# Kernel optimization log

Measured on AMD Instinct MI355X. Metric: run time of the kernel, lower is better.

The kernel has to match this reference:

```python
import jax, jax.numpy as jnp
import numpy as np


def setup_inputs() -> dict:
    key = jax.random.key(0)
    ks = jax.random.split(key, 6)
    B, N, D_in, D, Dg, H = 32, 256, 512, 256, 256, 512
    s = lambda f_in: 1.0 / np.sqrt(f_in)
    return {
        "xi": jax.random.normal(ks[0], (B, N, D_in), dtype=jnp.float32),
        "W_img": jax.random.normal(ks[1], (D_in, D), dtype=jnp.float32) * s(D_in),
        "b_img": jnp.zeros((D,), jnp.float32),
        "W_gnn_self": jax.random.normal(ks[2], (D, Dg), dtype=jnp.float32) * s(D),
        "W_gnn_nbr": jax.random.normal(ks[3], (D, Dg), dtype=jnp.float32) * s(D),
        "b_gnn": jnp.zeros((Dg,), jnp.float32),
        "W1": jax.random.normal(ks[4], (N * Dg, H), dtype=jnp.float32) * s(N * Dg),
        "b1": jnp.zeros((H,), jnp.float32),
        "W2": jax.random.normal(ks[5], (H, 1), dtype=jnp.float32) * s(H),
        "b2": jnp.zeros((1,), jnp.float32),
        "k": 10,
    }


def _knn_edges(xie, k):
    # xie: [B, N, D]. Per-image squared euclidean cdist + top-k (exclude self).
    B, N, _ = xie.shape
    x2 = jnp.sum(xie * xie, axis=-1)  # [B, N]
    d2 = x2[:, :, None] + x2[:, None, :] - 2.0 * jnp.einsum("bnd,bmd->bnm", xie, xie)
    big = jnp.asarray(1e30, d2.dtype)
    d2 = d2 + big * jnp.eye(N, dtype=d2.dtype)  # exclude self
    _, nbr = jax.lax.top_k(-d2, k)  # [B, N, k] neighbor (source) indices
    tgt = jnp.broadcast_to(jnp.arange(N)[None, :, None], (B, N, k))
    return nbr, tgt


def reference(xi, W_img, b_img, W_gnn_self, W_gnn_nbr, b_gnn, W1, b1, W2, b2, k):
    B, N, _ = xi.shape
    # image encoder -> per-node embeddings [B, N, D]
    xie = xi @ W_img + b_img
    # KNN graph build per image, then shift indices into one batched graph
    nbr, tgt = _knn_edges(xie, k)
    shift = (jnp.arange(B) * N)[:, None, None]
    src = (nbr + shift).reshape(-1)  # [B*N*k]
    dst = (tgt + shift).reshape(-1)  # [B*N*k]
    # batched graph conv: mean neighbor aggregation + self transform
    x_flat = xie.reshape(B * N, -1)
    agg = jax.ops.segment_sum(x_flat[src], dst, num_segments=B * N) / k
    gep = jax.nn.relu(x_flat @ W_gnn_self + agg @ W_gnn_nbr + b_gnn)
    gep = gep.reshape(B, N, -1)  # split_batch_graph
    # estimation MLP on flattened graph embedding
    h = jax.nn.relu(gep.reshape(B, -1) @ W1 + b1)
    out = h @ W2 + b2  # [B, 1]
    return xie, gep, out
```

## Files before the change

kernel.cpp:

```cpp
#include <hip/hip_runtime.h>

#define BB 32
#define NN 256
#define DIN 512
#define DD 256
#define HH 512
#define MM 8192
#define KSTR 16

typedef __attribute__((ext_vector_type(8))) __bf16 bf16x8;
typedef __attribute__((ext_vector_type(4))) float f32x4;
typedef unsigned short ushort_t;

__device__ __forceinline__ unsigned short f2bf(float x) {
  unsigned u = __float_as_uint(x);
  u += 0x7FFFu + ((u >> 16) & 1u);
  return (unsigned short)(u >> 16);
}

__global__ __launch_bounds__(512) void k_enc(const float* __restrict__ A,
                                             const float* __restrict__ W,
                                             const float* __restrict__ bias,
                                             float* __restrict__ C,
                                             ushort_t* __restrict__ A_bf) {
  __shared__ float Asm[32][520];
  const int tid = threadIdx.x;
  const int mb0 = blockIdx.x * 32;
  const int cg = tid & 31;
  const int mh = (tid >> 5) & 7;
  const int team = tid >> 8;
#pragma unroll
  for (int i = 0; i < 8; ++i) {
    int idx = tid + i * 512;
    int m = idx >> 7;
    int kq = idx & 127;
    float4 v = *reinterpret_cast<const float4*>(&A[(size_t)(mb0 + m) * DIN + kq * 4]);
    *reinterpret_cast<float4*>(&Asm[m][kq * 4]) = v;
  }
  __syncthreads();
  float4 acc[4][2] = {};
  const int kt0 = team * 256;
  const float* wp = &W[(size_t)kt0 * DD + cg * 8];
  float4 wA[4][2], wB[4][2];
#pragma unroll
  for (int j = 0; j < 4; ++j) {
    wA[j][0] = *reinterpret_cast<const float4*>(&wp[(size_t)j * DD]);
    wA[j][1] = *reinterpret_cast<const float4*>(&wp[(size_t)j * DD + 4]);
  }
  for (int it = 0; it < 64; ++it) {
    if (it < 63) {
#pragma unroll
      for (int j = 0; j < 4; ++j) {
        wB[j][0] = *reinterpret_cast<const float4*>(&wp[(size_t)((it + 1) * 4 + j) * DD]);
        wB[j][1] = *reinterpret_cast<const float4*>(&wp[(size_t)((it + 1) * 4 + j) * DD + 4]);
      }
    }
    const int kk = kt0 + it * 4;
#pragma unroll
    for (int r = 0; r < 4; ++r) {
      float4 a = *reinterpret_cast<const float4*>(&Asm[mh * 4 + r][kk]);
#pragma unroll
      for (int h = 0; h < 2; ++h) {
        acc[r][h].x += a.x * wA[0][h].x; acc[r][h].y += a.x * wA[0][h].y;
        acc[r][h].z += a.x * wA[0][h].z; acc[r][h].w += a.x * wA[0][h].w;
        acc[r][h].x += a.y * wA[1][h].x; acc[r][h].y += a.y * wA[1][h].y;
        acc[r][h].z += a.y * wA[1][h].z; acc[r][h].w += a.y * wA[1][h].w;
        acc[r][h].x += a.z * wA[2][h].x; acc[r][h].y += a.z * wA[2][h].y;
        acc[r][h].z += a.z * wA[2][h].z; acc[r][h].w += a.z * wA[2][h].w;
        acc[r][h].x += a.w * wA[3][h].x; acc[r][h].y += a.w * wA[3][h].y;
        acc[r][h].z += a.w * wA[3][h].z; acc[r][h].w += a.w * wA[3][h].w;
      }
    }
#pragma unroll
    for (int j = 0; j < 4; ++j) {
      wA[j][0] = wB[j][0]; wA[j][1] = wB[j][1];
    }
  }
  __syncthreads();
  float* red = &Asm[0][0];
  if (team == 1) {
#pragma unroll
    for (int r = 0; r < 4; ++r) {
      *reinterpret_cast<float4*>(&red[(mh * 4 + r) * 256 + cg * 8]) = acc[r][0];
      *reinterpret_cast<float4*>(&red[(mh * 4 + r) * 256 + cg * 8 + 4]) = acc[r][1];
    }
  }
  __syncthreads();
  if (team == 0) {
    float4 bv0 = *reinterpret_cast<const float4*>(&bias[cg * 8]);
    float4 bv1 = *reinterpret_cast<const float4*>(&bias[cg * 8 + 4]);
#pragma unroll
    for (int r = 0; r < 4; ++r) {
      const int row = mb0 + mh * 4 + r;
      float4 o0 = *reinterpret_cast<float4*>(&red[(mh * 4 + r) * 256 + cg * 8]);
      float4 o1 = *reinterpret_cast<float4*>(&red[(mh * 4 + r) * 256 + cg * 8 + 4]);
      float4 s0, s1;
      s0.x = acc[r][0].x + o0.x + bv0.x; s0.y = acc[r][0].y + o0.y + bv0.y;
      s0.z = acc[r][0].z + o0.z + bv0.z; s0.w = acc[r][0].w + o0.w + bv0.w;
      s1.x = acc[r][1].x + o1.x + bv1.x; s1.y = acc[r][1].y + o1.y + bv1.y;
      s1.z = acc[r][1].z + o1.z + bv1.z; s1.w = acc[r][1].w + o1.w + bv1.w;
      *reinterpret_cast<float4*>(&C[(size_t)row * DD + cg * 8]) = s0;
      *reinterpret_cast<float4*>(&C[(size_t)row * DD + cg * 8 + 4]) = s1;
      ushort4 ob0, ob1;
      ob0.x = f2bf(s0.x); ob0.y = f2bf(s0.y); ob0.z = f2bf(s0.z); ob0.w = f2bf(s0.w);
      ob1.x = f2bf(s1.x); ob1.y = f2bf(s1.y); ob1.z = f2bf(s1.z); ob1.w = f2bf(s1.w);
      *reinterpret_cast<ushort4*>(&A_bf[(size_t)row * 512 + cg * 8]) = ob0;
      *reinterpret_cast<ushort4*>(&A_bf[(size_t)row * 512 + cg * 8 + 4]) = ob1;
    }
  }
}

__global__ __launch_bounds__(256) void k_norm(const float* __restrict__ X,
                                              float* __restrict__ x2) {
  const int tid = threadIdx.x;
  const int row = blockIdx.x * 4 + (tid >> 6);
  const int lane = tid & 63;
  float4 v = *reinterpret_cast<const float4*>(&X[(size_t)row * DD + lane * 4]);
  float s = v.x * v.x + v.y * v.y + v.z * v.z + v.w * v.w;
#pragma unroll
  for (int off = 1; off < 64; off <<= 1) s += __shfl_xor(s, off);
  if (lane == 0) x2[row] = s;
}

__global__ __launch_bounds__(256) void k_dist(const float* __restrict__ X,
                                              const float* __restrict__ x2,
                                              float* __restrict__ d2) {
  __shared__ float As[16][68];
  __shared__ float Bs[16][68];
  const int tid = threadIdx.x;
  const int b = blockIdx.z;
  const int m0 = blockIdx.x * 64, n0 = blockIdx.y * 64;
  const float* Xb = X + b * NN * DD;
  const int tx = tid & 15, ty = tid >> 4;
  const int lrow = tid >> 2, lfc = (tid & 3) * 4;
  float acc[4][4] = {};
  for (int k0 = 0; k0 < DD; k0 += 16) {
    float4 va = *reinterpret_cast<const float4*>(&Xb[(n0 + lrow) * DD + k0 + lfc]);
    As[lfc + 0][lrow] = va.x; As[lfc + 1][lrow] = va.y;
    As[lfc + 2][lrow] = va.z; As[lfc + 3][lrow] = va.w;
    float4 vb = *reinterpret_cast<const float4*>(&Xb[(m0 + lrow) * DD + k0 + lfc]);
    Bs[lfc + 0][lrow] = vb.x; Bs[lfc + 1][lrow] = vb.y;
    Bs[lfc + 2][lrow] = vb.z; Bs[lfc + 3][lrow] = vb.w;
    __syncthreads();
#pragma unroll
    for (int kk = 0; kk < 16; ++kk) {
      float a[4], bv[4];
      *reinterpret_cast<float4*>(a) = *reinterpret_cast<float4*>(&As[kk][ty * 4]);
      *reinterpret_cast<float4*>(bv) = *reinterpret_cast<float4*>(&Bs[kk][tx * 4]);
#pragma unroll
      for (int i = 0; i < 4; ++i)
#pragma unroll
        for (int j = 0; j < 4; ++j) acc[i][j] += a[i] * bv[j];
    }
    __syncthreads();
  }
#pragma unroll
  for (int i = 0; i < 4; ++i) {
    const int n = n0 + ty * 4 + i;
    const float xn = x2[b * NN + n];
    float4 v;
    float* vv = reinterpret_cast<float*>(&v);
#pragma unroll
    for (int j = 0; j < 4; ++j) {
      const int mc = m0 + tx * 4 + j;
      float dv = xn + x2[b * NN + mc] - 2.0f * acc[i][j];
      if (n == mc) dv = 1e30f;
      vv[j] = dv;
    }
    *reinterpret_cast<float4*>(&d2[(size_t)(b * NN + n) * NN + m0 + tx * 4]) = v;
  }
}

__global__ __launch_bounds__(256) void k_topk(const float* __restrict__ d2,
                                              const int* __restrict__ kp,
                                              int* __restrict__ nbr) {
  const int tid = threadIdx.x;
  const int i = blockIdx.x * 4 + (tid >> 6);
  const int lane = tid & 63;
  const int kcnt = kp[0];
  const float* row = d2 + (size_t)i * NN;
  float v0 = row[lane];
  float v1 = row[lane + 64];
  float v2 = row[lane + 128];
  float v3 = row[lane + 192];
  for (int it = 0; it < kcnt; ++it) {
    float v = v0; int idx = lane;
    if (v1 < v) { v = v1; idx = lane + 64; }
    if (v2 < v) { v = v2; idx = lane + 128; }
    if (v3 < v) { v = v3; idx = lane + 192; }
#pragma unroll
    for (int off = 1; off < 64; off <<= 1) {
      float ov = __shfl_xor(v, off);
      int oi = __shfl_xor(idx, off);
      if (ov < v || (ov == v && oi < idx)) { v = ov; idx = oi; }
    }
    if (lane == 0) nbr[i * KSTR + it] = idx;
    const int slot = idx >> 6;
    if (lane == (idx & 63)) {
      if (slot == 0) v0 = 3e38f;
      else if (slot == 1) v1 = 3e38f;
      else if (slot == 2) v2 = 3e38f;
      else v3 = 3e38f;
    }
  }
}

__global__ __launch_bounds__(256) void k_agg(const float* __restrict__ X,
                                             const int* __restrict__ nbr,
                                             const int* __restrict__ kp,
                                             ushort_t* __restrict__ A_bf) {
  const int i = blockIdx.x;
  const int b = i >> 8;
  const int t = threadIdx.x;
  const int kcnt = kp[0];
  float acc = 0.0f;
  for (int j = 0; j < kcnt; ++j) {
    const int nb = nbr[i * KSTR + j];
    acc += X[(size_t)(b * NN + nb) * DD + t];
  }
  A_bf[(size_t)i * 512 + 256 + t] = f2bf(acc / (float)kcnt);
}

__global__ __launch_bounds__(256) void k_cvtw(const float* __restrict__ Ws,
                                              const float* __restrict__ Wn,
                                              ushort_t* __restrict__ B_bfT) {
  const int id = blockIdx.x * 256 + threadIdx.x;
  const int k = id >> 8;
  const int n = id & 255;
  float v = (k < 256) ? Ws[(size_t)k * 256 + n] : Wn[(size_t)(k - 256) * 256 + n];
  B_bfT[(size_t)n * 512 + k] = f2bf(v);
}

__global__ __launch_bounds__(256) void k_gnn(const ushort_t* __restrict__ A_bf,
                                             const ushort_t* __restrict__ B_bfT,
                                             const float* __restrict__ bias,
                                             float* __restrict__ C,
                                             ushort_t* __restrict__ gep_bf) {
  __shared__ ushort_t As[64 * 72];
  __shared__ ushort_t Bs[64 * 72];
  const int tid = threadIdx.x;
  const int m0 = blockIdx.x * 64, n0 = blockIdx.y * 64;
  const int l = tid & 63, w = tid >> 6;
  const int mw = (w & 1) * 32, nw = (w >> 1) * 32;
  const int lr = tid >> 3, lq = tid & 7;
  f32x4 acc[2][2] = {};
  for (int kt = 0; kt < 8; ++kt) {
    const int kb = kt * 64;
#pragma unroll
    for (int s = 0; s < 2; ++s) {
      const int r = lr + s * 32;
      uint4 va = *reinterpret_cast<const uint4*>(&A_bf[(size_t)(m0 + r) * 512 + kb + lq * 8]);
      *reinterpret_cast<uint4*>(&As[r * 72 + lq * 8]) = va;
      uint4 vb = *reinterpret_cast<const uint4*>(&B_bfT[(size_t)(n0 + r) * 512 + kb + lq * 8]);
      *reinterpret_cast<uint4*>(&Bs[r * 72 + lq * 8]) = vb;
    }
    __syncthreads();
#pragma unroll
    for (int ks = 0; ks < 2; ++ks) {
      bf16x8 af[2], bf[2];
#pragma unroll
      for (int mi = 0; mi < 2; ++mi)
        af[mi] = *reinterpret_cast<const bf16x8*>(
            &As[(mw + mi * 16 + (l & 15)) * 72 + ks * 32 + (l >> 4) * 8]);
#pragma unroll
      for (int ni = 0; ni < 2; ++ni)
        bf[ni] = *reinterpret_cast<const bf16x8*>(
            &Bs[(nw + ni * 16 + (l & 15)) * 72 + ks * 32 + (l >> 4) * 8]);
#pragma unroll
      for (int mi = 0; mi < 2; ++mi)
#pragma unroll
        for (int ni = 0; ni < 2; ++ni)
          acc[mi][ni] = __builtin_amdgcn_mfma_f32_16x16x32_bf16(af[mi], bf[ni],
                                                                acc[mi][ni], 0, 0, 0);
    }
    __syncthreads();
  }
#pragma unroll
  for (int mi = 0; mi < 2; ++mi) {
    const int row_base = m0 + mw + mi * 16 + (l >> 4) * 4;
#pragma unroll
    for (int ni = 0; ni < 2; ++ni) {
      const int col = n0 + nw + ni * 16 + (l & 15);
      const float bv = bias[col];
#pragma unroll
      for (int r = 0; r < 4; ++r) {
        float v = acc[mi][ni][r] + bv;
        v = v > 0.0f ? v : 0.0f;
        C[(size_t)(row_base + r) * 256 + col] = v;
        gep_bf[(size_t)(row_base + r) * 256 + col] = f2bf(v);
      }
    }
  }
}

__global__ __launch_bounds__(512) void k_mlp1(const ushort_t* __restrict__ gep_bf,
                                              const float* __restrict__ W1,
                                              float* __restrict__ part) {
  __shared__ ushort_t WbT[2][512][40];
  __shared__ ushort_t Ab[32][264];
  const int tid = threadIdx.x;
  const int b = blockIdx.x;
  const int l = tid & 63, w = tid >> 6;
#pragma unroll
  for (int i = 0; i < 2; ++i) {
    int id = tid + i * 512;
    int m = id >> 5, dq8 = (id & 31) * 8;
    *reinterpret_cast<uint4*>(&Ab[m][dq8]) = *reinterpret_cast<const uint4*>(
        &gep_bf[((size_t)m * 256 + b) * 256 + dq8]);
  }
  const float* Wbase = W1 + (size_t)b * 256 * 512 + tid;
  float wreg[32];
  auto WLOAD = [&](int s) {
#pragma unroll
    for (int kk = 0; kk < 32; ++kk)
      wreg[kk] = Wbase[(size_t)(s * 32 + kk) * 512];
  };
  auto WSTORE = [&](int buf) {
#pragma unroll
    for (int q = 0; q < 4; ++q) {
      ushort_t tmp[8];
#pragma unroll
      for (int j = 0; j < 8; ++j) tmp[j] = f2bf(wreg[q * 8 + j]);
      *reinterpret_cast<uint4*>(&WbT[buf][tid][q * 8]) =
          *reinterpret_cast<const uint4*>(tmp);
    }
  };
  WLOAD(0);
  WSTORE(0);
  __syncthreads();
  const int n0w = w * 64;
  f32x4 acc[2][4] = {};
  for (int s = 0; s < 8; ++s) {
    const int cur = s & 1;
    if (s < 7) WLOAD(s + 1);
    bf16x8 a[2], bw[4];
#pragma unroll
    for (int mi = 0; mi < 2; ++mi)
      a[mi] = *reinterpret_cast<const bf16x8*>(
          &Ab[mi * 16 + (l & 15)][s * 32 + (l >> 4) * 8]);
#pragma unroll
    for (int nf = 0; nf < 4; ++nf)
      bw[nf] = *reinterpret_cast<const bf16x8*>(
          &WbT[cur][n0w + nf * 16 + (l & 15)][(l >> 4) * 8]);
#pragma unroll
    for (int mi = 0; mi < 2; ++mi)
#pragma unroll
      for (int nf = 0; nf < 4; ++nf)
        acc[mi][nf] = __builtin_amdgcn_mfma_f32_16x16x32_bf16(a[mi], bw[nf],
                                                              acc[mi][nf], 0, 0, 0);
    if (s < 7) {
      WSTORE(cur ^ 1);
      __syncthreads();
    }
  }
#pragma unroll
  for (int mi = 0; mi < 2; ++mi)
#pragma unroll
    for (int nf = 0; nf < 4; ++nf) {
      const int col = n0w + nf * 16 + (l & 15);
#pragma unroll
      for (int r = 0; r < 4; ++r) {
        const int m = mi * 16 + (l >> 4) * 4 + r;
        part[((size_t)b * 32 + m) * HH + col] = acc[mi][nf][r];
      }
    }
}

__global__ __launch_bounds__(256) void k_fin(const float* __restrict__ part,
                                             const float* __restrict__ b1,
                                             const float* __restrict__ W2,
                                             const float* __restrict__ b2,
                                             float* __restrict__ outp) {
  __shared__ float red[4];
  const int tid = threadIdx.x;
  const int m = blockIdx.x;
  const int c0 = tid * 2;
  float s0 = 0.f, s1 = 0.f, s2 = 0.f, s3 = 0.f;
  for (int bb = 0; bb < 256; bb += 2) {
    float2 v0 = *reinterpret_cast<const float2*>(&part[((size_t)bb * 32 + m) * 512 + c0]);
    float2 v1 = *reinterpret_cast<const float2*>(&part[((size_t)(bb + 1) * 32 + m) * 512 + c0]);
    s0 += v0.x; s1 += v0.y; s2 += v1.x; s3 += v1.y;
  }
  float h0 = s0 + s2 + b1[c0];
  float h1 = s1 + s3 + b1[c0 + 1];
  h0 = h0 > 0.f ? h0 : 0.f;
  h1 = h1 > 0.f ? h1 : 0.f;
  float val = h0 * W2[c0] + h1 * W2[c0 + 1];
#pragma unroll
  for (int off = 1; off < 64; off <<= 1) val += __shfl_xor(val, off);
  const int w = tid >> 6;
  if ((tid & 63) == 0) red[w] = val;
  __syncthreads();
  if (tid == 0) outp[m] = red[0] + red[1] + red[2] + red[3] + b2[0];
}

extern "C" void kernel_launch(void* const* d_in, const int* in_sizes, int n_in,
                              void* d_out, int out_size, void* d_ws, size_t ws_size,
                              hipStream_t stream) {
  const float* xi     = (const float*)d_in[0];
  const float* W_img  = (const float*)d_in[1];
  const float* b_img  = (const float*)d_in[2];
  const float* W_self = (const float*)d_in[3];
  const float* W_nbr  = (const float*)d_in[4];
  const float* b_gnn  = (const float*)d_in[5];
  const float* W1     = (const float*)d_in[6];
  const float* b1     = (const float*)d_in[7];
  const float* W2     = (const float*)d_in[8];
  const float* b2     = (const float*)d_in[9];
  const int*   kp     = (const int*)d_in[10];

  float* xie  = (float*)d_out;
  float* gep  = xie + (size_t)MM * DD;
  float* outp = gep + (size_t)MM * DD;

  float* ws   = (float*)d_ws;
  float* x2   = ws;
  int*   nbr  = (int*)(ws + 8192);
  float* d2   = ws + 8192 + 131072;
  float* part = d2 + (size_t)2097152;
  ushort_t* A_bf   = (ushort_t*)(part + 4194304);
  ushort_t* B_bfT  = A_bf + (size_t)MM * 512;
  ushort_t* gep_bf = B_bfT + 131072;

  k_enc  <<<MM / 32, 512, 0, stream>>>(xi, W_img, b_img, xie, A_bf);
  k_cvtw <<<512, 256, 0, stream>>>(W_self, W_nbr, B_bfT);
  k_norm <<<MM / 4, 256, 0, stream>>>(xie, x2);
  k_dist <<<dim3(4, 4, BB), 256, 0, stream>>>(xie, x2, d2);
  k_topk <<<MM / 4, 256, 0, stream>>>(d2, kp, nbr);
  k_agg  <<<MM, 256, 0, stream>>>(xie, nbr, kp, A_bf);
  k_gnn  <<<dim3(128, 4), 256, 0, stream>>>(A_bf, B_bfT, b_gnn, gep, gep_bf);
  k_mlp1 <<<256, 512, 0, stream>>>(gep_bf, W1, part);
  k_fin  <<<BB, 256, 0, stream>>>(part, b1, W2, b2, outp);
}
```

Baseline: 152.6 us.

## Fuse top-k with aggregation, restructure distance GEMM and GNN GEMM tiling

The encoder now also writes a transposed copy of xie so the distance kernel can stream it as a register-prefetched weight matrix, with a 32-row A tile in shared memory and 256 blocks of 512 threads. Top-k selection and neighbor mean aggregation are fused into one kernel that keeps the indices in shared memory and gathers with float4 loads, which removes the global nbr buffer and one launch. The GNN GEMM moves to 128x64 tiles filled by direct global-to-LDS loads. In exchange there is an extra 8 MB transposed write in the encoder, and the new LDS layout drops the row padding, which may cause bank conflicts.

```diff
diff --git a/kernel.cpp b/kernel.cpp
--- a/kernel.cpp
+++ b/kernel.cpp
@@ -12,6 +12,10 @@
 typedef __attribute__((ext_vector_type(4))) float f32x4;
 typedef unsigned short ushort_t;
 
+typedef const float __attribute__((address_space(1)))* gas1f;
+typedef const unsigned int __attribute__((address_space(1)))* gas1u;
+typedef unsigned int __attribute__((address_space(3)))* las3u;
+
 __device__ __forceinline__ unsigned short f2bf(float x) {
   unsigned u = __float_as_uint(x);
   u += 0x7FFFu + ((u >> 16) & 1u);
@@ -22,7 +26,8 @@
                                              const float* __restrict__ W,
                                              const float* __restrict__ bias,
                                              float* __restrict__ C,
-                                             ushort_t* __restrict__ A_bf) {
+                                             ushort_t* __restrict__ A_bf,
+                                             float* __restrict__ xieT) {
   __shared__ float Asm[32][520];
   const int tid = threadIdx.x;
   const int mb0 = blockIdx.x * 32;
@@ -106,7 +111,23 @@
       ob1.x = f2bf(s1.x); ob1.y = f2bf(s1.y); ob1.z = f2bf(s1.z); ob1.w = f2bf(s1.w);
       *reinterpret_cast<ushort4*>(&A_bf[(size_t)row * 512 + cg * 8]) = ob0;
       *reinterpret_cast<ushort4*>(&A_bf[(size_t)row * 512 + cg * 8 + 4]) = ob1;
-    }
+      *reinterpret_cast<float4*>(&red[(mh * 4 + r) * 256 + cg * 8]) = s0;
+      *reinterpret_cast<float4*>(&red[(mh * 4 + r) * 256 + cg * 8 + 4]) = s1;
+    }
+  }
+  __syncthreads();
+  {
+    const int b = mb0 >> 8;
+    const int n0b = mb0 & 255;
+    const int d = tid >> 1;
+    const int nh = (tid & 1) * 16;
+    float tmp[16];
+#pragma unroll
+    for (int i = 0; i < 16; ++i) tmp[i] = red[(nh + i) * 256 + d];
+    float* dst = &xieT[((size_t)b * 256 + d) * 256 + n0b + nh];
+#pragma unroll
+    for (int i = 0; i < 4; ++i)
+      *reinterpret_cast<float4*>(&dst[i * 4]) = *reinterpret_cast<float4*>(&tmp[i * 4]);
   }
 }
 
@@ -122,60 +143,92 @@
   if (lane == 0) x2[row] = s;
 }
 
-__global__ __launch_bounds__(256) void k_dist(const float* __restrict__ X,
-                                              const float* __restrict__ x2,
+__global__ __launch_bounds__(512) void k_dist(const float* __restrict__ xie,
+                                              const float* __restrict__ xieT,
+                                              const float* __restrict__ x2g,
                                               float* __restrict__ d2) {
-  __shared__ float As[16][68];
-  __shared__ float Bs[16][68];
-  const int tid = threadIdx.x;
-  const int b = blockIdx.z;
-  const int m0 = blockIdx.x * 64, n0 = blockIdx.y * 64;
-  const float* Xb = X + b * NN * DD;
-  const int tx = tid & 15, ty = tid >> 4;
-  const int lrow = tid >> 2, lfc = (tid & 3) * 4;
-  float acc[4][4] = {};
-  for (int k0 = 0; k0 < DD; k0 += 16) {
-    float4 va = *reinterpret_cast<const float4*>(&Xb[(n0 + lrow) * DD + k0 + lfc]);
-    As[lfc + 0][lrow] = va.x; As[lfc + 1][lrow] = va.y;
-    As[lfc + 2][lrow] = va.z; As[lfc + 3][lrow] = va.w;
-    float4 vb = *reinterpret_cast<const float4*>(&Xb[(m0 + lrow) * DD + k0 + lfc]);
-    Bs[lfc + 0][lrow] = vb.x; Bs[lfc + 1][lrow] = vb.y;
-    Bs[lfc + 2][lrow] = vb.z; Bs[lfc + 3][lrow] = vb.w;
-    __syncthreads();
-#pragma unroll
-    for (int kk = 0; kk < 16; ++kk) {
-      float a[4], bv[4];
-      *reinterpret_cast<float4*>(a) = *reinterpret_cast<float4*>(&As[kk][ty * 4]);
-      *reinterpret_cast<float4*>(bv) = *reinterpret_cast<float4*>(&Bs[kk][tx * 4]);
-#pragma unroll
-      for (int i = 0; i < 4; ++i)
-#pragma unroll
-        for (int j = 0; j < 4; ++j) acc[i][j] += a[i] * bv[j];
-    }
-    __syncthreads();
-  }
+  __shared__ float Asm[32][260];
+  const int tid = threadIdx.x;
+  const int b = blockIdx.x >> 3;
+  const int n0b = (blockIdx.x & 7) * 32;
+  const int base = b * 256;
+  const int cg = tid & 31;
+  const int rg = tid >> 5;
 #pragma unroll
   for (int i = 0; i < 4; ++i) {
-    const int n = n0 + ty * 4 + i;
-    const float xn = x2[b * NN + n];
-    float4 v;
-    float* vv = reinterpret_cast<float*>(&v);
+    int idx = tid + i * 512;
+    int m = idx >> 6;
+    int kq = idx & 63;
+    float4 v = *reinterpret_cast<const float4*>(
+        &xie[(size_t)(base + n0b + m) * DD + kq * 4]);
+    *reinterpret_cast<float4*>(&Asm[m][kq * 4]) = v;
+  }
+  __syncthreads();
+  float4 acc[2][2] = {};
+  const float* wp = &xieT[(size_t)base * 256 + cg * 8];
+  float4 wA[4][2], wB[4][2];
+#pragma unroll
+  for (int j = 0; j < 4; ++j) {
+    wA[j][0] = *reinterpret_cast<const float4*>(&wp[(size_t)j * 256]);
+    wA[j][1] = *reinterpret_cast<const float4*>(&wp[(size_t)j * 256 + 4]);
+  }
+  for (int it = 0; it < 64; ++it) {
+    if (it < 63) {
+#pragma unroll
+      for (int j = 0; j < 4; ++j) {
+        wB[j][0] = *reinterpret_cast<const float4*>(&wp[(size_t)((it + 1) * 4 + j) * 256]);
+        wB[j][1] = *reinterpret_cast<const float4*>(&wp[(size_t)((it + 1) * 4 + j) * 256 + 4]);
+      }
+    }
+#pragma unroll
+    for (int r = 0; r < 2; ++r) {
+      float4 a = *reinterpret_cast<const float4*>(&Asm[rg * 2 + r][it * 4]);
+#pragma unroll
+      for (int h = 0; h < 2; ++h) {
+        acc[r][h].x += a.x * wA[0][h].x; acc[r][h].y += a.x * wA[0][h].y;
+        acc[r][h].z += a.x * wA[0][h].z; acc[r][h].w += a.x * wA[0][h].w;
+        acc[r][h].x += a.y * wA[1][h].x; acc[r][h].y += a.y * wA[1][h].y;
+        acc[r][h].z += a.y * wA[1][h].z; acc[r][h].w += a.y * wA[1][h].w;
+        acc[r][h].x += a.z * wA[2][h].x; acc[r][h].y += a.z * wA[2][h].y;
+        acc[r][h].z += a.z * wA[2][h].z; acc[r][h].w += a.z * wA[2][h].w;
+        acc[r][h].x += a.w * wA[3][h].x; acc[r][h].y += a.w * wA[3][h].y;
+        acc[r][h].z += a.w * wA[3][h].z; acc[r][h].w += a.w * wA[3][h].w;
+      }
+    }
 #pragma unroll
     for (int j = 0; j < 4; ++j) {
-      const int mc = m0 + tx * 4 + j;
-      float dv = xn + x2[b * NN + mc] - 2.0f * acc[i][j];
-      if (n == mc) dv = 1e30f;
-      vv[j] = dv;
-    }
-    *reinterpret_cast<float4*>(&d2[(size_t)(b * NN + n) * NN + m0 + tx * 4]) = v;
-  }
-}
-
-__global__ __launch_bounds__(256) void k_topk(const float* __restrict__ d2,
-                                              const int* __restrict__ kp,
-                                              int* __restrict__ nbr) {
-  const int tid = threadIdx.x;
-  const int i = blockIdx.x * 4 + (tid >> 6);
+      wA[j][0] = wB[j][0]; wA[j][1] = wB[j][1];
+    }
+  }
+#pragma unroll
+  for (int r = 0; r < 2; ++r) {
+    const int nl = n0b + rg * 2 + r;
+    const float xn = x2g[base + nl];
+#pragma unroll
+    for (int h = 0; h < 2; ++h) {
+      const float* accp = reinterpret_cast<const float*>(&acc[r][h]);
+      float4 v;
+      float* vv = reinterpret_cast<float*>(&v);
+#pragma unroll
+      for (int j2 = 0; j2 < 4; ++j2) {
+        const int mc = cg * 8 + h * 4 + j2;
+        float dv = xn + x2g[base + mc] - 2.0f * accp[j2];
+        if (nl == mc) dv = 1e30f;
+        vv[j2] = dv;
+      }
+      *reinterpret_cast<float4*>(&d2[(size_t)(base + nl) * 256 + cg * 8 + h * 4]) = v;
+    }
+  }
+}
+
+__global__ __launch_bounds__(256) void k_topkagg(const float* __restrict__ X,
+                                                 const float* __restrict__ d2,
+                                                 const int* __restrict__ kp,
+                                                 ushort_t* __restrict__ A_bf) {
+  __shared__ int nbrL[4][KSTR];
+  const int tid = threadIdx.x;
+  const int rw = tid >> 6;
+  const int i = blockIdx.x * 4 + rw;
   const int lane = tid & 63;
   const int kcnt = kp[0];
   const float* row = d2 + (size_t)i * NN;
@@ -194,7 +247,7 @@
       int oi = __shfl_xor(idx, off);
       if (ov < v || (ov == v && oi < idx)) { v = ov; idx = oi; }
     }
-    if (lane == 0) nbr[i * KSTR + it] = idx;
+    if (lane == 0) nbrL[rw][it] = idx;
     const int slot = idx >> 6;
     if (lane == (idx & 63)) {
       if (slot == 0) v0 = 3e38f;
@@ -203,22 +256,22 @@
       else v3 = 3e38f;
     }
   }
-}
-
-__global__ __launch_bounds__(256) void k_agg(const float* __restrict__ X,
-                                             const int* __restrict__ nbr,
-                                             const int* __restrict__ kp,
-                                             ushort_t* __restrict__ A_bf) {
-  const int i = blockIdx.x;
-  const int b = i >> 8;
-  const int t = threadIdx.x;
-  const int kcnt = kp[0];
-  float acc = 0.0f;
-  for (int j = 0; j < kcnt; ++j) {
-    const int nb = nbr[i * KSTR + j];
-    acc += X[(size_t)(b * NN + nb) * DD + t];
-  }
-  A_bf[(size_t)i * 512 + 256 + t] = f2bf(acc / (float)kcnt);
+  __syncthreads();
+  {
+    const int b = i >> 8;
+    float4 s = make_float4(0.f, 0.f, 0.f, 0.f);
+    for (int j = 0; j < kcnt; ++j) {
+      const int nb = nbrL[rw][j];
+      float4 v = *reinterpret_cast<const float4*>(
+          &X[(size_t)(b * NN + nb) * DD + lane * 4]);
+      s.x += v.x; s.y += v.y; s.z += v.z; s.w += v.w;
+    }
+    const float sc = 1.0f / (float)kcnt;
+    ushort4 ob;
+    ob.x = f2bf(s.x * sc); ob.y = f2bf(s.y * sc);
+    ob.z = f2bf(s.z * sc); ob.w = f2bf(s.w * sc);
+    *reinterpret_cast<ushort4*>(&A_bf[(size_t)i * 512 + 256 + lane * 4]) = ob;
+  }
 }
 
 __global__ __launch_bounds__(256) void k_cvtw(const float* __restrict__ Ws,
@@ -236,48 +289,52 @@
                                              const float* __restrict__ bias,
                                              float* __restrict__ C,
                                              ushort_t* __restrict__ gep_bf) {
-  __shared__ ushort_t As[64 * 72];
-  __shared__ ushort_t Bs[64 * 72];
-  const int tid = threadIdx.x;
-  const int m0 = blockIdx.x * 64, n0 = blockIdx.y * 64;
+  __shared__ ushort_t As[128 * 64];
+  __shared__ ushort_t Bs[64 * 64];
+  const int tid = threadIdx.x;
+  const int m0 = blockIdx.x * 128, n0 = blockIdx.y * 64;
   const int l = tid & 63, w = tid >> 6;
-  const int mw = (w & 1) * 32, nw = (w >> 1) * 32;
-  const int lr = tid >> 3, lq = tid & 7;
-  f32x4 acc[2][2] = {};
+  const int mw = (w & 1) * 64, nw = (w >> 1) * 32;
+  f32x4 acc[4][2] = {};
   for (int kt = 0; kt < 8; ++kt) {
     const int kb = kt * 64;
-#pragma unroll
-    for (int s = 0; s < 2; ++s) {
-      const int r = lr + s * 32;
-      uint4 va = *reinterpret_cast<const uint4*>(&A_bf[(size_t)(m0 + r) * 512 + kb + lq * 8]);
-      *reinterpret_cast<uint4*>(&As[r * 72 + lq * 8]) = va;
-      uint4 vb = *reinterpret_cast<const uint4*>(&B_bfT[(size_t)(n0 + r) * 512 + kb + lq * 8]);
-      *reinterpret_cast<uint4*>(&Bs[r * 72 + lq * 8]) = vb;
+    const int grow = w * 8 + (l >> 3);
+    const int gcol = (l & 7) * 8;
+#pragma unroll
+    for (int it2 = 0; it2 < 4; ++it2) {
+      __builtin_amdgcn_global_load_lds(
+          (gas1u)&A_bf[(size_t)(m0 + it2 * 32 + grow) * 512 + kb + gcol],
+          (las3u)((char*)As + it2 * 4096 + w * 1024), 16, 0, 0);
+    }
+#pragma unroll
+    for (int it2 = 0; it2 < 2; ++it2) {
+      __builtin_amdgcn_global_load_lds(
+          (gas1u)&B_bfT[(size_t)(n0 + it2 * 32 + grow) * 512 + kb + gcol],
+          (las3u)((char*)Bs + it2 * 4096 + w * 1024), 16, 0, 0);
     }
     __syncthreads();
 #pragma unroll
     for (int ks = 0; ks < 2; ++ks) {
-      bf16x8 af[2], bf[2];
-#pragma unroll
-      for (int mi = 0; mi < 2; ++mi)
-        af[mi] = *reinterpret_cast<const bf16x8*>(
-            &As[(mw + mi * 16 + (l & 15)) * 72 + ks * 32 + (l >> 4) * 8]);
+      const int koff = ks * 32 + (l >> 4) * 8;
+      bf16x8 a[4], bv[2];
+#pragma unroll
+      for (int mi = 0; mi < 4; ++mi)
+        a[mi] = *reinterpret_cast<const bf16x8*>(&As[(mw + mi * 16 + (l & 15)) * 64 + koff]);
 #pragma unroll
       for (int ni = 0; ni < 2; ++ni)
-        bf[ni] = *reinterpret_cast<const bf16x8*>(
-            &Bs[(nw + ni * 16 + (l & 15)) * 72 + ks * 32 + (l >> 4) * 8]);
-#pragma unroll
-      for (int mi = 0; mi < 2; ++mi)
+        bv[ni] = *reinterpret_cast<const bf16x8*>(&Bs[(nw + ni * 16 + (l & 15)) * 64 + koff]);
+#pragma unroll
+      for (int mi = 0; mi < 4; ++mi)
 #pragma unroll
         for (int ni = 0; ni < 2; ++ni)
-          acc[mi][ni] = __builtin_amdgcn_mfma_f32_16x16x32_bf16(af[mi], bf[ni],
+          acc[mi][ni] = __builtin_amdgcn_mfma_f32_16x16x32_bf16(a[mi], bv[ni],
                                                                 acc[mi][ni], 0, 0, 0);
     }
     __syncthreads();
   }
 #pragma unroll
-  for (int mi = 0; mi < 2; ++mi) {
-    const int row_base = m0 + mw + mi * 16 + (l >> 4) * 4;
+  for (int mi = 0; mi < 4; ++mi) {
+    const int rb = m0 + mw + mi * 16 + (l >> 4) * 4;
 #pragma unroll
     for (int ni = 0; ni < 2; ++ni) {
       const int col = n0 + nw + ni * 16 + (l & 15);
@@ -286,8 +343,8 @@
       for (int r = 0; r < 4; ++r) {
         float v = acc[mi][ni][r] + bv;
         v = v > 0.0f ? v : 0.0f;
-        C[(size_t)(row_base + r) * 256 + col] = v;
-        gep_bf[(size_t)(row_base + r) * 256 + col] = f2bf(v);
+        C[(size_t)(rb + r) * 256 + col] = v;
+        gep_bf[(size_t)(rb + r) * 256 + col] = f2bf(v);
       }
     }
   }
@@ -415,20 +472,19 @@
 
   float* ws   = (float*)d_ws;
   float* x2   = ws;
-  int*   nbr  = (int*)(ws + 8192);
-  float* d2   = ws + 8192 + 131072;
+  float* d2   = ws + 8192;
   float* part = d2 + (size_t)2097152;
-  ushort_t* A_bf   = (ushort_t*)(part + 4194304);
+  float* xieT = part + (size_t)4194304;
+  ushort_t* A_bf   = (ushort_t*)(xieT + 2097152);
   ushort_t* B_bfT  = A_bf + (size_t)MM * 512;
   ushort_t* gep_bf = B_bfT + 131072;
 
-  k_enc  <<<MM / 32, 512, 0, stream>>>(xi, W_img, b_img, xie, A_bf);
-  k_cvtw <<<512, 256, 0, stream>>>(W_self, W_nbr, B_bfT);
-  k_norm <<<MM / 4, 256, 0, stream>>>(xie, x2);
-  k_dist <<<dim3(4, 4, BB), 256, 0, stream>>>(xie, x2, d2);
-  k_topk <<<MM / 4, 256, 0, stream>>>(d2, kp, nbr);
-  k_agg  <<<MM, 256, 0, stream>>>(xie, nbr, kp, A_bf);
-  k_gnn  <<<dim3(128, 4), 256, 0, stream>>>(A_bf, B_bfT, b_gnn, gep, gep_bf);
-  k_mlp1 <<<256, 512, 0, stream>>>(gep_bf, W1, part);
-  k_fin  <<<BB, 256, 0, stream>>>(part, b1, W2, b2, outp);
-}
+  k_enc    <<<MM / 32, 512, 0, stream>>>(xi, W_img, b_img, xie, A_bf, xieT);
+  k_cvtw   <<<512, 256, 0, stream>>>(W_self, W_nbr, B_bfT);
+  k_norm   <<<MM / 4, 256, 0, stream>>>(xie, x2);
+  k_dist   <<<256, 512, 0, stream>>>(xie, xieT, x2, d2);
+  k_topkagg<<<MM / 4, 256, 0, stream>>>(xie, d2, kp, A_bf);
+  k_gnn    <<<dim3(64, 4), 256, 0, stream>>>(A_bf, B_bfT, b_gnn, gep, gep_bf);
+  k_mlp1   <<<256, 512, 0, stream>>>(gep_bf, W1, part);
+  k_fin    <<<BB, 256, 0, stream>>>(part, b1, W2, b2, outp);
+}
```

Result: no change. 153.2 us (+0.4%).
